# Kernel tuning notes

Measured on AMD Instinct MI355X. Metric: run time of the kernel, lower is better.

The kernel has to match this reference:

```python
import jax, jax.numpy as jnp
import numpy as np

I = 512  # input_size
H = 512  # hidden_size
B = 64   # batch
S = 512  # seq_len


def _lstm_dir(x_sbi, U, W, b, reverse):
    """Run one LSTM direction over time.
    x_sbi: [S,B,I]; U: [4,H,H]; W: [4,I,H]; b: [4,H] (gate order f,g,i,o).
    Returns hs: [S,B,H] in original time order.
    """
    # Precompute input projections for all timesteps/gates: [S,4,B,H]
    xw = jnp.einsum('sbi,gih->sgbh', x_sbi, W) + b[None, :, None, :]

    def step(carry, xw_t):
        h, c = carry
        f = jax.nn.sigmoid(h @ U[0] + xw_t[0])
        g = jnp.tanh(h @ U[1] + xw_t[1])
        i = jax.nn.sigmoid(h @ U[2] + xw_t[2])
        c = c * f + g * i
        o = jax.nn.sigmoid(h @ U[3] + xw_t[3])
        h = o * jnp.tanh(c)
        return (h, c), h

    h0 = jnp.zeros((x_sbi.shape[1], U.shape[-1]), dtype=x_sbi.dtype)
    (_, _), hs = jax.lax.scan(step, (h0, h0), xw, reverse=reverse)
    return hs  # scan with reverse=True already emits outputs in original order


def setup_inputs() -> dict:
    key = jax.random.key(0)
    ks = jax.random.split(key, 7)
    u = lambda k, shp: jax.random.uniform(k, shp, jnp.float32, -0.1, 0.1)
    return {
        'x': jax.random.normal(ks[0], (B, S, I), jnp.float32),
        'mask': jnp.ones((B, S), dtype=bool),
        'U_fwd': u(ks[1], (4, H, H)),
        'W_fwd': u(ks[2], (4, I, H)),
        'b_fwd': u(ks[3], (4, H)),
        'U_bwd': u(ks[4], (4, H, H)),
        'W_bwd': u(ks[5], (4, I, H)),
        'b_bwd': u(ks[6], (4, H)),
    }


def reference(x, mask, U_fwd, W_fwd, b_fwd, U_bwd, W_bwd, b_bwd):
    # x: [B,S,I] batch-first -> time-major [S,B,I] (matches torch permute(1,0,2))
    x_sbi = jnp.transpose(x, (1, 0, 2))
    fwd = _lstm_dir(x_sbi, U_fwd, W_fwd, b_fwd, reverse=False)  # [S,B,H]
    bwd = _lstm_dir(x_sbi, U_bwd, W_bwd, b_bwd, reverse=True)   # [S,B,H]
    output = jnp.concatenate([fwd, bwd], axis=-1)  # [S,B,2H] (time-major, like original)
    lengths = mask.sum(axis=1).astype(jnp.int32)
    fwd_idx = jnp.clip(lengths - 1, 0, None)
    bidx = jnp.arange(x.shape[0])
    h_f = fwd[fwd_idx, bidx]  # [B,H]
    h_b = bwd[0, bidx]        # [B,H]
    return output, h_f, h_b
```

## Files before the change

kernel.cpp:

```cpp
#include <hip/hip_runtime.h>
#include <math.h>


#define Sd 512
#define Bd 64
#define Hd 512
#define TWO_H 1024

typedef __attribute__((ext_vector_type(8))) short bf16x8;
typedef __attribute__((ext_vector_type(4))) float f32x4;

#define UWT_OFF   0u
#define BIAS_OFF  8388608u
#define HBF_OFF   8404992u
#define FLG_OFF   8667136u
#define XT_OFF    8668160u
#define WS_NEED   (XT_OFF + 33554432u)

__device__ __forceinline__ unsigned short f2bf(float f) {
    unsigned u = __float_as_uint(f);
    u += 0x7fffu + ((u >> 16) & 1u);
    return (unsigned short)(u >> 16);
}
__device__ __forceinline__ float sigmoidf_(float v) { return 1.0f / (1.0f + __expf(-v)); }
__device__ __forceinline__ float tanhf_(float v) {
    const float e = __expf(2.0f * v);
    return 1.0f - 2.0f / (e + 1.0f);
}
__device__ __forceinline__ unsigned cvt_pk_bf16(float lo, float hi) {
    unsigned r;
    asm("v_cvt_pk_bf16_f32 %0, %1, %2" : "=v"(r) : "v"(lo), "v"(hi));
    return r;
}
__device__ __forceinline__ void gld_lds16(const void* g, void* l) {
    __builtin_amdgcn_global_load_lds(
        (const __attribute__((address_space(1))) void*)(g),
        (__attribute__((address_space(3))) void*)(l), 16, 0, 0);
}
__device__ __forceinline__ void raw_bar() {
    __builtin_amdgcn_sched_barrier(0);
    __builtin_amdgcn_s_barrier();
    __builtin_amdgcn_sched_barrier(0);
}
__device__ __forceinline__ void lgkm_bar() {
    asm volatile("s_waitcnt lgkmcnt(0)" ::: "memory");
    raw_bar();
}

#define LDH4(d0, d1, d2, d3, base)                                          \
    asm volatile("global_load_dwordx4 %0, %4, off sc0 sc1\n\t"              \
                 "global_load_dwordx4 %1, %4, off offset:1024 sc0 sc1\n\t"  \
                 "global_load_dwordx4 %2, %4, off offset:2048 sc0 sc1\n\t"  \
                 "global_load_dwordx4 %3, %4, off offset:3072 sc0 sc1"      \
                 : "=&v"(d0), "=&v"(d1), "=&v"(d2), "=&v"(d3)               \
                 : "v"(base))

__global__ __launch_bounds__(256) void prep_weights(
    const float* __restrict__ U_f, const float* __restrict__ W_f,
    const float* __restrict__ U_b, const float* __restrict__ W_b,
    unsigned short* __restrict__ uwt)
{
    const unsigned i = blockIdx.x * 256u + threadIdx.x;
    const int h   = i & 511;
    const int k8  = (i >> 9) & 63;
    const int g   = (i >> 15) & 3;
    const int mat = (i >> 17) & 1;
    const int d   = (i >> 18) & 1;

    const float* src = mat ? (d ? W_b : W_f) : (d ? U_b : U_f);
    src += (size_t)g * Hd * Hd + (size_t)(k8 * 8) * Hd + h;

    const int n    = h * 4 + g;
    const int nt   = n >> 4;
    const int lane = (n & 15) + ((mat * 64 + k8) & 3) * 16;
    const int kb   = mat * 16 + (k8 >> 2);

    bf16x8 v;
    #pragma unroll
    for (int j = 0; j < 8; ++j)
        v[j] = (short)f2bf(src[(size_t)j * Hd]);

    ((bf16x8*)uwt)[((d * 128 + nt) * 32 + kb) * 64 + lane] = v;
}

__global__ __launch_bounds__(256) void prep_x(
    const float* __restrict__ x, unsigned short* __restrict__ xt)
{
    const unsigned i = blockIdx.x * 256u + threadIdx.x;
    const int v  = i & 2047;
    const int t  = (i >> 11) & 511;
    const int mh = (i >> 20) & 1;
    const int m  = v >> 6;
    const int w  = (v & 63) ^ (m & 7);
    const int k0 = (w >> 2) * 32 + (w & 3) * 8;
    const int b  = mh * 32 + m;
    const float4* s = (const float4*)(x + ((size_t)b * Sd + t) * Hd + k0);
    const float4 u0 = s[0], u1 = s[1];
    bf16x8 o;
    unsigned* ou = (unsigned*)&o;
    ou[0] = cvt_pk_bf16(u0.x, u0.y); ou[1] = cvt_pk_bf16(u0.z, u0.w);
    ou[2] = cvt_pk_bf16(u1.x, u1.y); ou[3] = cvt_pk_bf16(u1.z, u1.w);
    ((bf16x8*)xt)[i] = o;
}

__global__ __launch_bounds__(256) void prep_misc(
    const float* __restrict__ b_f, const float* __restrict__ b_b,
    unsigned char* __restrict__ ws)
{
    const unsigned i = blockIdx.x * 256u + threadIdx.x;
    ((int4*)(ws + HBF_OFF))[i] = make_int4(0, 0, 0, 0);
    if (i < 4096) {
        const int d = i >> 11;
        const int n = i & 2047;
        const int g = n & 3;
        const int h = n >> 2;
        ((float*)(ws + BIAS_OFF))[i] = (d ? b_b : b_f)[g * Hd + h];
    }
    if (i < 256) ((unsigned*)(ws + FLG_OFF))[i] = 0u;
}

template<bool XT>
__global__ __launch_bounds__(256, 1) void lstm_persist(
    const float* __restrict__ x,
    unsigned char* __restrict__ ws,
    float* __restrict__ out)
{
    const int blk   = blockIdx.x;
    const int g     = blk & 3;
    const int d     = g & 1;
    const int mhalf = (g >> 1) & 1;
    const int ng    = blk >> 2;
    const int tid   = threadIdx.x;
    const int wid   = tid >> 6;
    const int lane  = tid & 63;

    const bf16x8* uwt_v = (const bf16x8*)(ws + UWT_OFF);
    bf16x8*       hbf_w = (bf16x8*)(ws + HBF_OFF);
    const float*  biasp = (const float*)(ws + BIAS_OFF);
    unsigned*     flg   = (unsigned*)(ws + FLG_OFF) + (size_t)g * 64;
    const char*   xt    = (const char*)(ws + XT_OFF);

    __shared__ __align__(16) short xs[16640];
    __shared__ __align__(16) float gbuf[32 * 64];
    __shared__ float hbuf[32 * 16];

    const int nt  = ng * 4 + wid;
    const int mt0 = mhalf * 2;

    bf16x8 Bfrag[32];
    {
        const bf16x8* Bp = uwt_v + (size_t)((d * 128 + nt) * 32) * 64 + lane;
        #pragma unroll
        for (int kb = 0; kb < 32; ++kb) Bfrag[kb] = Bp[(size_t)kb * 64];
    }

    const int jloc = tid & 15;
    const int mloc = tid >> 4;
    const float* bias = biasp + d * 2048 + ng * 64 + jloc * 4;
    const float bf_ = bias[0], bg_ = bias[1], bi_ = bias[2], bo_ = bias[3];

    float c0 = 0.f, c1 = 0.f;
    const float4* x4 = (const float4*)x;
    const int r0 = lane & 15, q = lane >> 4, r07 = r0 & 7;
    const bf16x8* xv = (const bf16x8*)xs;
    char* xsb = (char*)xs;

    f32x4 xacc0, xacc1;
    bf16x8 A0[16], A1[16];

    auto stage_x = [&](int tn) {
        const char* tb = xt + ((size_t)(mhalf * 512 + tn) * 2048) * 16;
        #pragma unroll
        for (int j = 0; j < 8; ++j) {
            const int chunk = wid * 8 + j;
            gld_lds16(tb + (size_t)chunk * 1024 + (size_t)lane * 16,
                      xsb + chunk * 1024);
        }
    };
    auto stage_x_conv = [&](int tn) {
        for (int i = tid; i < 32 * 128; i += 256) {
            const int m  = i >> 7;
            const int c4 = i & 127;
            const int b  = mhalf * 32 + m;
            const float4 v = x4[((size_t)b * Sd + tn) * 128 + c4];
            short* p = xs + m * 520 + c4 * 4;
            *(uint2*)p = make_uint2(cvt_pk_bf16(v.x, v.y), cvt_pk_bf16(v.z, v.w));
        }
    };
    auto xmfma = [&]() {
        xacc0 = (f32x4){0.f, 0.f, 0.f, 0.f};
        xacc1 = (f32x4){0.f, 0.f, 0.f, 0.f};
        #pragma unroll
        for (int kb2 = 0; kb2 < 16; ++kb2) {
            const bf16x8 bfrag = Bfrag[16 + kb2];
            int u0, u1;
            if constexpr (XT) { u0 = r0 * 64 + ((kb2 * 4 + q) ^ r07); u1 = u0 + 1024; }
            else              { u0 = r0 * 65 + kb2 * 4 + q;           u1 = u0 + 16 * 65; }
            const bf16x8 a0 = xv[u0];
            const bf16x8 a1 = xv[u1];
            xacc0 = __builtin_amdgcn_mfma_f32_16x16x32_bf16(a0, bfrag, xacc0, 0, 0, 0);
            xacc1 = __builtin_amdgcn_mfma_f32_16x16x32_bf16(a1, bfrag, xacc1, 0, 0, 0);
        }
    };
    auto issue_h = [&](int p) {
        const unsigned char* hb = ws + HBF_OFF
            + ((size_t)(((p * 2 + d) * 4 + mt0) * 16) * 64 + lane) * 16;
        LDH4(A0[0],  A0[1],  A0[2],  A0[3],  hb);
        LDH4(A0[4],  A0[5],  A0[6],  A0[7],  hb + 4096);
        LDH4(A0[8],  A0[9],  A0[10], A0[11], hb + 8192);
        LDH4(A0[12], A0[13], A0[14], A0[15], hb + 12288);
        LDH4(A1[0],  A1[1],  A1[2],  A1[3],  hb + 16384);
        LDH4(A1[4],  A1[5],  A1[6],  A1[7],  hb + 20480);
        LDH4(A1[8],  A1[9],  A1[10], A1[11], hb + 24576);
        LDH4(A1[12], A1[13], A1[14], A1[15], hb + 28672);
    };

    {
        const int t0 = d ? (Sd - 1) : 0;
        if constexpr (XT) {
            stage_x(t0);
            asm volatile("s_waitcnt vmcnt(0)" ::: "memory");
        } else {
            stage_x_conv(t0);
        }
    }
    __syncthreads();
    xmfma();
    issue_h(0);

    for (int t = 0; t < Sd; ++t) {
        const int t_orig = d ? (Sd - 1 - t) : t;
        const int p1 = (t & 1) ^ 1;

        if constexpr (XT) {
            raw_bar();
            const int tn = d ? ((Sd - 2 - t) > 0 ? (Sd - 2 - t) : 0)
                             : ((t + 1) < (Sd - 1) ? (t + 1) : (Sd - 1));
            stage_x(tn);
        }

        f32x4 acc0 = xacc0, acc1 = xacc1;
        if constexpr (XT) asm volatile("s_waitcnt vmcnt(24)" ::: "memory");
        else              asm volatile("s_waitcnt vmcnt(16)" ::: "memory");
        __builtin_amdgcn_sched_barrier(0);
        #pragma unroll
        for (int kb = 0; kb < 16; ++kb)
            acc0 = __builtin_amdgcn_mfma_f32_16x16x32_bf16(A0[kb], Bfrag[kb], acc0, 0, 0, 0);
        __builtin_amdgcn_sched_barrier(0);
        if constexpr (XT) asm volatile("s_waitcnt vmcnt(8)" ::: "memory");
        else              asm volatile("s_waitcnt vmcnt(0)" ::: "memory");
        __builtin_amdgcn_sched_barrier(0);
        #pragma unroll
        for (int kb = 0; kb < 16; ++kb)
            acc1 = __builtin_amdgcn_mfma_f32_16x16x32_bf16(A1[kb], Bfrag[kb], acc1, 0, 0, 0);

        {
            const int nl = wid * 16 + (lane & 15);
            const int mr = (lane >> 4) * 4;
            #pragma unroll
            for (int r = 0; r < 4; ++r) gbuf[(mr + r) * 64 + nl] = acc0[r];
            #pragma unroll
            for (int r = 0; r < 4; ++r) gbuf[(16 + mr + r) * 64 + nl] = acc1[r];
        }
        lgkm_bar();

        float h0c, h1c;
        {
            const f32x4 ga = *(const f32x4*)&gbuf[mloc * 64 + jloc * 4];
            const f32x4 gb = *(const f32x4*)&gbuf[(mloc + 16) * 64 + jloc * 4];
            c0 = c0 * sigmoidf_(ga[0] + bf_) + tanhf_(ga[1] + bg_) * sigmoidf_(ga[2] + bi_);
            h0c = sigmoidf_(ga[3] + bo_) * tanhf_(c0);
            c1 = c1 * sigmoidf_(gb[0] + bf_) + tanhf_(gb[1] + bg_) * sigmoidf_(gb[2] + bi_);
            h1c = sigmoidf_(gb[3] + bo_) * tanhf_(c1);
            hbuf[mloc * 16 + jloc] = h0c;
            hbuf[(mloc + 16) * 16 + jloc] = h1c;
        }
        lgkm_bar();

        if (t < Sd - 1) {
            if (tid < 64) {
                const int ml2 = tid >> 1;
                const int jh  = tid & 1;
                const int b   = mhalf * 32 + ml2;
                const int jb  = ng * 16 + jh * 8;
                const int kb  = jb >> 5;
                const int lq  = (jb >> 3) & 3;
                const int lh  = (b & 15) + lq * 16;
                const int mt  = b >> 4;
                const float* hp4 = &hbuf[ml2 * 16 + jh * 8];
                bf16x8 v;
                unsigned* vu = (unsigned*)&v;
                vu[0] = cvt_pk_bf16(hp4[0], hp4[1]);
                vu[1] = cvt_pk_bf16(hp4[2], hp4[3]);
                vu[2] = cvt_pk_bf16(hp4[4], hp4[5]);
                vu[3] = cvt_pk_bf16(hp4[6], hp4[7]);
                bf16x8* hp = hbf_w + (size_t)(((p1 * 2 + d) * 4 + mt) * 16 + kb) * 64 + lh;
                asm volatile("global_store_dwordx4 %0, %1, off sc0 sc1"
                             :: "v"(hp), "v"(v) : "memory");
                asm volatile("s_waitcnt vmcnt(0)" ::: "memory");
                if (tid == 0) {
                    unsigned* fp = flg + ng;
                    const unsigned fv = (unsigned)(t + 1);
                    asm volatile("global_store_dword %0, %1, off sc0 sc1"
                                 :: "v"(fp), "v"(fv) : "memory");
                }
            }
            {
                const unsigned tgt = (unsigned)(t + 1);
                const unsigned* fp = flg + (lane & 31);
                int guard = 0;
                for (;;) {
                    unsigned v;
                    asm volatile("global_load_dword %0, %1, off sc0 sc1\n\t"
                                 "s_waitcnt vmcnt(0)"
                                 : "=v"(v) : "v"(fp) : "memory");
                    if (__ballot(v >= tgt) == ~0ull) break;
                    __builtin_amdgcn_s_sleep(1);
                    if (++guard > (1 << 15)) break;
                }
                __builtin_amdgcn_sched_barrier(0);
            }
        }

        {
            const int b0 = mhalf * 32 + mloc;
            const int jg = ng * 16 + jloc;
            float* ob = out + (size_t)d * Hd + jg;
            __builtin_nontemporal_store(h0c, ob + ((size_t)t_orig * Bd + b0) * TWO_H);
            __builtin_nontemporal_store(h1c, ob + ((size_t)t_orig * Bd + b0 + 16) * TWO_H);
            if (t == Sd - 1) {
                float* hf = out + (size_t)Sd * Bd * TWO_H + (size_t)d * Bd * Hd + jg;
                hf[(size_t)b0 * Hd] = h0c;
                hf[(size_t)(b0 + 16) * Hd] = h1c;
            }
        }

        if (t == Sd - 1) break;

        issue_h(p1);

        if constexpr (XT) {
            asm volatile("s_waitcnt vmcnt(32)" ::: "memory");
            __builtin_amdgcn_sched_barrier(0);
            raw_bar();
        } else {
            const int tn = d ? (Sd - 2 - t) : (t + 1);
            stage_x_conv(tn);
            lgkm_bar();
        }
        xmfma();
    }
}

extern "C" void kernel_launch(void* const* d_in, const int* in_sizes, int n_in,
                              void* d_out, int out_size, void* d_ws, size_t ws_size,
                              hipStream_t stream) {
    const float* x   = (const float*)d_in[0];
    const float* U_f = (const float*)d_in[2];
    const float* W_f = (const float*)d_in[3];
    const float* b_f = (const float*)d_in[4];
    const float* U_b = (const float*)d_in[5];
    const float* W_b = (const float*)d_in[6];
    const float* b_b = (const float*)d_in[7];
    float* out = (float*)d_out;
    unsigned char* ws = (unsigned char*)d_ws;

    prep_weights<<<2048, 256, 0, stream>>>(U_f, W_f, U_b, W_b,
                                           (unsigned short*)(ws + UWT_OFF));
    prep_misc<<<64, 256, 0, stream>>>(b_f, b_b, ws);

    if (ws_size >= (size_t)WS_NEED) {
        prep_x<<<8192, 256, 0, stream>>>(x, (unsigned short*)(ws + XT_OFF));
        lstm_persist<true><<<128, 256, 0, stream>>>(x, ws, out);
    } else {
        lstm_persist<false><<<128, 256, 0, stream>>>(x, ws, out);
    }
}
```

Before: 2.484 ms.

## Replace flag-based step sync with data-validity polling over an 8-slot hidden ring

Adds a new persistent LSTM kernel that exchanges the bf16 hidden state through an 8-slot ring in global memory. Consumers detect readiness by checking that the loaded fragments are nonzero and reissue the loads if not, instead of waiting on per-step flags. A lagging progress counter guards clearing of ring slots three steps ahead. The aim is to drop the flag round-trip from the per-timestep critical path. The risk is that a legitimate h value of exactly zero in bf16 would spin until the guard limit, and the correctness of the scheme rests on that assumption plus bounded retry guards.

```diff
diff --git a/kernel.cpp b/kernel.cpp
--- a/kernel.cpp
+++ b/kernel.cpp
@@ -12,10 +12,14 @@
 
 #define UWT_OFF   0u
 #define BIAS_OFF  8388608u
+#define RING_OFF  8404992u
+#define PRG_OFF   9453568u
+#define XT0_OFF   9455616u
+#define WS_NEED0  (XT0_OFF + 33554432u)
 #define HBF_OFF   8404992u
 #define FLG_OFF   8667136u
-#define XT_OFF    8668160u
-#define WS_NEED   (XT_OFF + 33554432u)
+#define XT1_OFF   8668160u
+#define WS_NEED1  (XT1_OFF + 33554432u)
 
 __device__ __forceinline__ unsigned short f2bf(float f) {
     unsigned u = __float_as_uint(f);
@@ -45,6 +49,13 @@
 __device__ __forceinline__ void lgkm_bar() {
     asm volatile("s_waitcnt lgkmcnt(0)" ::: "memory");
     raw_bar();
+}
+__device__ __forceinline__ bool frag_ok(const bf16x8& f) {
+    union { bf16x8 v; unsigned u[4]; } w; w.v = f;
+    unsigned a = w.u[0] < w.u[1] ? w.u[0] : w.u[1];
+    unsigned b = w.u[2] < w.u[3] ? w.u[2] : w.u[3];
+    a = a < b ? a : b;
+    return a != 0u;
 }
 
 #define LDH4(d0, d1, d2, d3, base)                                          \
@@ -105,10 +116,11 @@
 
 __global__ __launch_bounds__(256) void prep_misc(
     const float* __restrict__ b_f, const float* __restrict__ b_b,
-    unsigned char* __restrict__ ws)
+    unsigned char* __restrict__ ws, unsigned long long zero_bytes)
 {
     const unsigned i = blockIdx.x * 256u + threadIdx.x;
-    ((int4*)(ws + HBF_OFF))[i] = make_int4(0, 0, 0, 0);
+    if ((unsigned long long)i * 16ull < zero_bytes)
+        ((int4*)(ws + RING_OFF))[i] = make_int4(0, 0, 0, 0);
     if (i < 4096) {
         const int d = i >> 11;
         const int n = i & 2047;
@@ -116,11 +128,235 @@
         const int h = n >> 2;
         ((float*)(ws + BIAS_OFF))[i] = (d ? b_b : b_f)[g * Hd + h];
     }
-    if (i < 256) ((unsigned*)(ws + FLG_OFF))[i] = 0u;
+}
+
+__global__ __launch_bounds__(256, 1) void lstm_data(
+    unsigned char* __restrict__ ws,
+    float* __restrict__ out)
+{
+    const int blk   = blockIdx.x;
+    const int g     = blk & 3;
+    const int d     = g & 1;
+    const int mhalf = (g >> 1) & 1;
+    const int ng    = blk >> 2;
+    const int tid   = threadIdx.x;
+    const int wid   = tid >> 6;
+    const int lane  = tid & 63;
+
+    const bf16x8* uwt_v = (const bf16x8*)(ws + UWT_OFF);
+    bf16x8*       ring  = (bf16x8*)(ws + RING_OFF);
+    int*          prg   = (int*)(ws + PRG_OFF) + g * 32;
+    const float*  biasp = (const float*)(ws + BIAS_OFF);
+    const char*   xt    = (const char*)(ws + XT0_OFF);
+
+    __shared__ __align__(16) short xs[16384];
+    __shared__ __align__(16) float gbuf[32 * 64];
+    __shared__ float hbuf[32 * 16];
+
+    const int nt = ng * 4 + wid;
+
+    bf16x8 Bfrag[32];
+    {
+        const bf16x8* Bp = uwt_v + (size_t)((d * 128 + nt) * 32) * 64 + lane;
+        #pragma unroll
+        for (int kb = 0; kb < 32; ++kb) Bfrag[kb] = Bp[(size_t)kb * 64];
+    }
+
+    const int jloc = tid & 15;
+    const int mloc = tid >> 4;
+    const float* bias = biasp + d * 2048 + ng * 64 + jloc * 4;
+    const float bf_ = bias[0], bg_ = bias[1], bi_ = bias[2], bo_ = bias[3];
+
+    float c0 = 0.f, c1 = 0.f;
+    const int r0 = lane & 15, q = lane >> 4, r07 = r0 & 7;
+    const bf16x8* xv = (const bf16x8*)xs;
+    char* xsb = (char*)xs;
+
+    f32x4 xacc0, xacc1;
+    bf16x8 A0[16], A1[16];
+    #pragma unroll
+    for (int i = 0; i < 16; ++i) { A0[i] = (bf16x8)(short)0; A1[i] = (bf16x8)(short)0; }
+
+    auto stage_x = [&](int tn) {
+        const char* tb = xt + ((size_t)(mhalf * 512 + tn) * 2048) * 16;
+        #pragma unroll
+        for (int j = 0; j < 8; ++j) {
+            const int chunk = wid * 8 + j;
+            gld_lds16(tb + (size_t)chunk * 1024 + (size_t)lane * 16,
+                      xsb + chunk * 1024);
+        }
+    };
+    auto xmfma = [&]() {
+        xacc0 = (f32x4){0.f, 0.f, 0.f, 0.f};
+        xacc1 = (f32x4){0.f, 0.f, 0.f, 0.f};
+        #pragma unroll
+        for (int kb2 = 0; kb2 < 16; ++kb2) {
+            const bf16x8 bfrag = Bfrag[16 + kb2];
+            const int u0 = r0 * 64 + ((kb2 * 4 + q) ^ r07);
+            const bf16x8 a0 = xv[u0];
+            const bf16x8 a1 = xv[u0 + 1024];
+            xacc0 = __builtin_amdgcn_mfma_f32_16x16x32_bf16(a0, bfrag, xacc0, 0, 0, 0);
+            xacc1 = __builtin_amdgcn_mfma_f32_16x16x32_bf16(a1, bfrag, xacc1, 0, 0, 0);
+        }
+    };
+    auto issue_h = [&](int slot) {
+        const unsigned char* hb = (const unsigned char*)(ring
+            + (size_t)((slot & 7) * 4 + g) * 2048 + lane);
+        LDH4(A0[0],  A0[1],  A0[2],  A0[3],  hb);
+        LDH4(A0[4],  A0[5],  A0[6],  A0[7],  hb + 4096);
+        LDH4(A0[8],  A0[9],  A0[10], A0[11], hb + 8192);
+        LDH4(A0[12], A0[13], A0[14], A0[15], hb + 12288);
+        LDH4(A1[0],  A1[1],  A1[2],  A1[3],  hb + 16384);
+        LDH4(A1[4],  A1[5],  A1[6],  A1[7],  hb + 20480);
+        LDH4(A1[8],  A1[9],  A1[10], A1[11], hb + 24576);
+        LDH4(A1[12], A1[13], A1[14], A1[15], hb + 28672);
+    };
+
+    {
+        const int t0 = d ? (Sd - 1) : 0;
+        stage_x(t0);
+        asm volatile("s_waitcnt vmcnt(0)" ::: "memory");
+        __builtin_amdgcn_sched_barrier(0);
+    }
+    __syncthreads();
+    xmfma();
+
+    for (int t = 0; t < Sd; ++t) {
+        const int t_orig = d ? (Sd - 1 - t) : t;
+
+        f32x4 acc0 = xacc0, acc1 = xacc1;
+        #pragma unroll
+        for (int kb = 0; kb < 16; ++kb) {
+            acc0 = __builtin_amdgcn_mfma_f32_16x16x32_bf16(A0[kb], Bfrag[kb], acc0, 0, 0, 0);
+            acc1 = __builtin_amdgcn_mfma_f32_16x16x32_bf16(A1[kb], Bfrag[kb], acc1, 0, 0, 0);
+        }
+
+        {
+            const int nl = wid * 16 + (lane & 15);
+            const int mr = (lane >> 4) * 4;
+            #pragma unroll
+            for (int r = 0; r < 4; ++r) gbuf[(mr + r) * 64 + nl] = acc0[r];
+            #pragma unroll
+            for (int r = 0; r < 4; ++r) gbuf[(16 + mr + r) * 64 + nl] = acc1[r];
+        }
+        lgkm_bar();
+
+        float h0c, h1c;
+        {
+            const f32x4 ga = *(const f32x4*)&gbuf[mloc * 64 + jloc * 4];
+            const f32x4 gb = *(const f32x4*)&gbuf[(mloc + 16) * 64 + jloc * 4];
+            c0 = c0 * sigmoidf_(ga[0] + bf_) + tanhf_(ga[1] + bg_) * sigmoidf_(ga[2] + bi_);
+            h0c = sigmoidf_(ga[3] + bo_) * tanhf_(c0);
+            c1 = c1 * sigmoidf_(gb[0] + bf_) + tanhf_(gb[1] + bg_) * sigmoidf_(gb[2] + bi_);
+            h1c = sigmoidf_(gb[3] + bo_) * tanhf_(c1);
+        }
+
+        if (t == Sd - 1) {
+            const int b0 = mhalf * 32 + mloc;
+            const int jg = ng * 16 + jloc;
+            float* ob = out + (size_t)d * Hd + jg;
+            __builtin_nontemporal_store(h0c, ob + ((size_t)t_orig * Bd + b0) * TWO_H);
+            __builtin_nontemporal_store(h1c, ob + ((size_t)t_orig * Bd + b0 + 16) * TWO_H);
+            float* hf = out + (size_t)Sd * Bd * TWO_H + (size_t)d * Bd * Hd + jg;
+            hf[(size_t)b0 * Hd] = h0c;
+            hf[(size_t)(b0 + 16) * Hd] = h1c;
+            break;
+        }
+
+        hbuf[mloc * 16 + jloc] = h0c;
+        hbuf[(mloc + 16) * 16 + jloc] = h1c;
+        lgkm_bar();
+
+        if (wid == 0) {
+            const int ml2 = lane >> 1;
+            const int jh  = lane & 1;
+            const int jb  = ng * 16 + jh * 8;
+            const int kb  = jb >> 5;
+            const int lq  = (jb >> 3) & 3;
+            const int lh  = (ml2 & 15) + lq * 16;
+            const int mtl = ml2 >> 4;
+            const float* hp4 = &hbuf[ml2 * 16 + jh * 8];
+            bf16x8 v;
+            unsigned* vu = (unsigned*)&v;
+            vu[0] = cvt_pk_bf16(hp4[0], hp4[1]);
+            vu[1] = cvt_pk_bf16(hp4[2], hp4[3]);
+            vu[2] = cvt_pk_bf16(hp4[4], hp4[5]);
+            vu[3] = cvt_pk_bf16(hp4[6], hp4[7]);
+            bf16x8* hp = ring + (size_t)(((t + 1) & 7) * 4 + g) * 2048
+                       + (mtl * 16 + kb) * 64 + lh;
+            asm volatile("global_store_dwordx4 %0, %1, off sc0 sc1"
+                         :: "v"(hp), "v"(v) : "memory");
+            if (lane == 0) {
+                int* pp = prg + ng;
+                const int pv = t + 1;
+                asm volatile("global_store_dword %0, %1, off sc0 sc1"
+                             :: "v"(pp), "v"(pv) : "memory");
+            }
+        }
+
+        if (wid == 1) {
+            {
+                const int* pp = prg + (lane & 31);
+                int guard = 0;
+                for (;;) {
+                    int v;
+                    asm volatile("global_load_dword %0, %1, off sc0 sc1\n\t"
+                                 "s_waitcnt vmcnt(0)"
+                                 : "=v"(v) : "v"(pp) : "memory");
+                    if (__ballot(v >= t - 3) == ~0ull) break;
+                    __builtin_amdgcn_s_sleep(1);
+                    if (++guard > (1 << 13)) break;
+                }
+            }
+            const int ml2 = lane >> 1;
+            const int jh  = lane & 1;
+            const int jb  = ng * 16 + jh * 8;
+            const int kb  = jb >> 5;
+            const int lq  = (jb >> 3) & 3;
+            const int lh  = (ml2 & 15) + lq * 16;
+            const int mtl = ml2 >> 4;
+            bf16x8* zp = ring + (size_t)(((t + 3) & 7) * 4 + g) * 2048
+                       + (mtl * 16 + kb) * 64 + lh;
+            const bf16x8 z = (bf16x8)(short)0;
+            asm volatile("global_store_dwordx4 %0, %1, off sc0 sc1"
+                         :: "v"(zp), "v"(z) : "memory");
+        }
+
+        {
+            const int b0 = mhalf * 32 + mloc;
+            const int jg = ng * 16 + jloc;
+            float* ob = out + (size_t)d * Hd + jg;
+            __builtin_nontemporal_store(h0c, ob + ((size_t)t_orig * Bd + b0) * TWO_H);
+            __builtin_nontemporal_store(h1c, ob + ((size_t)t_orig * Bd + b0 + 16) * TWO_H);
+        }
+
+        stage_x(d ? (Sd - 2 - t) : (t + 1));
+        issue_h(t + 1);
+
+        asm volatile("s_waitcnt vmcnt(32)" ::: "memory");
+        __builtin_amdgcn_sched_barrier(0);
+        raw_bar();
+        xmfma();
+
+        {
+            int guard = 0;
+            for (;;) {
+                asm volatile("s_waitcnt vmcnt(0)" ::: "memory");
+                __builtin_amdgcn_sched_barrier(0);
+                bool ok = true;
+                #pragma unroll
+                for (int i = 0; i < 16; ++i) { ok &= frag_ok(A0[i]); ok &= frag_ok(A1[i]); }
+                if (__ballot(ok) == ~0ull) break;
+                if (++guard > (1 << 12)) break;
+                issue_h(t + 1);
+            }
+            __builtin_amdgcn_sched_barrier(0);
+        }
+    }
 }
 
 template<bool XT>
-__global__ __launch_bounds__(256, 1) void lstm_persist(
+__global__ __launch_bounds__(256, 1) void lstm_flag(
     const float* __restrict__ x,
     unsigned char* __restrict__ ws,
     float* __restrict__ out)
@@ -138,7 +374,7 @@
     bf16x8*       hbf_w = (bf16x8*)(ws + HBF_OFF);
     const float*  biasp = (const float*)(ws + BIAS_OFF);
     unsigned*     flg   = (unsigned*)(ws + FLG_OFF) + (size_t)g * 64;
-    const char*   xt    = (const char*)(ws + XT_OFF);
+    const char*   xt    = (const char*)(ws + XT1_OFF);
 
     __shared__ __align__(16) short xs[16640];
     __shared__ __align__(16) float gbuf[32 * 64];
@@ -367,12 +603,17 @@
 
     prep_weights<<<2048, 256, 0, stream>>>(U_f, W_f, U_b, W_b,
                                            (unsigned short*)(ws + UWT_OFF));
-    prep_misc<<<64, 256, 0, stream>>>(b_f, b_b, ws);
-
-    if (ws_size >= (size_t)WS_NEED) {
-        prep_x<<<8192, 256, 0, stream>>>(x, (unsigned short*)(ws + XT_OFF));
-        lstm_persist<true><<<128, 256, 0, stream>>>(x, ws, out);
+
+    if (ws_size >= (size_t)WS_NEED0) {
+        prep_misc<<<260, 256, 0, stream>>>(b_f, b_b, ws, 1050624ull);
+        prep_x<<<8192, 256, 0, stream>>>(x, (unsigned short*)(ws + XT0_OFF));
+        lstm_data<<<128, 256, 0, stream>>>(ws, out);
+    } else if (ws_size >= (size_t)WS_NEED1) {
+        prep_misc<<<66, 256, 0, stream>>>(b_f, b_b, ws, 264192ull);
+        prep_x<<<8192, 256, 0, stream>>>(x, (unsigned short*)(ws + XT1_OFF));
+        lstm_flag<true><<<128, 256, 0, stream>>>(x, ws, out);
     } else {
-        lstm_persist<false><<<128, 256, 0, stream>>>(x, ws, out);
-    }
-}
+        prep_misc<<<66, 256, 0, stream>>>(b_f, b_b, ws, 264192ull);
+        lstm_flag<false><<<128, 256, 0, stream>>>(x, ws, out);
+    }
+}
```

After: 3.184 ms. 1.28x slower.
